# Performance work log

Hardware: AMD Instinct MI355X
Metric: run time of the kernel (lower is better)

The kernel has to match this reference:

```python
import jax, jax.numpy as jnp
import numpy as np

EMB = 1024
HEADS = 16
WINDOW = 128


def setup_inputs() -> dict:
    key = jax.random.key(0)
    ks = jax.random.split(key, 9)
    B, N = 2, 2048
    s = 0.02
    f32 = jnp.float32
    return {
        "x": jax.random.normal(ks[0], (B, N, EMB), dtype=f32),
        "Wq": jax.random.normal(ks[1], (EMB, EMB), dtype=f32) * s,
        "bq": jnp.zeros((EMB,), dtype=f32),
        "Wk": jax.random.normal(ks[2], (EMB, EMB), dtype=f32) * s,
        "bk": jnp.zeros((EMB,), dtype=f32),
        "Wv": jax.random.normal(ks[3], (EMB, EMB), dtype=f32) * s,
        "bv": jnp.zeros((EMB,), dtype=f32),
        "Wp": jax.random.normal(ks[4], (EMB, EMB), dtype=f32) * s,
        "bp": jnp.zeros((EMB,), dtype=f32),
    }


def reference(x, Wq, bq, Wk, bk, Wv, bv, Wp, bp):
    B, N, E = x.shape
    H = HEADS
    d = E // H

    def proj(W, b):
        # torch nn.Linear: y = x @ W^T + b, then split heads -> [b, h, n, d]
        y = jnp.einsum('bne,fe->bnf', x, W) + b
        return y.reshape(B, N, H, d).transpose(0, 2, 1, 3)

    q = proj(Wq, bq)
    k = proj(Wk, bk)
    v = proj(Wv, bv)

    # full QK^T then mask out-of-window entries (faithful to original)
    energy = jnp.einsum('bhqd,bhkd->bhqk', q, k)  # [B,H,N,N]
    idx = jnp.arange(N)
    out_of_window = jnp.abs(idx[:, None] - idx[None, :]) > WINDOW  # [N,N] bool
    fmin = jnp.finfo(jnp.float32).min
    energy = jnp.where(out_of_window, fmin, energy)

    scaling = jnp.sqrt(jnp.float32(E))  # note: original scales by sqrt(emb_size)
    att = jax.nn.softmax(energy / scaling, axis=-1)

    out = jnp.einsum('bhqk,bhkd->bhqd', att, v)  # [B,H,N,d]
    out = out.transpose(0, 2, 1, 3).reshape(B, N, E)
    return jnp.einsum('bne,fe->bnf', out, Wp) + bp
```

## Files before the change

kernel.cpp:

```cpp
#include <hip/hip_runtime.h>
#include <stdint.h>

#define EMB    1024
#define NHEAD  16
#define HDIM   64
#define NSEQ   2048
#define NBATCH 2
#define WINDOW 128
#define MROWS  (NBATCH * NSEQ)

typedef __attribute__((ext_vector_type(8))) short  bf16x8;
typedef __attribute__((ext_vector_type(4))) float  f32x4;
typedef __attribute__((ext_vector_type(4))) short  short4v;

__device__ __forceinline__ unsigned short f2bf(float f) {
  union { float f; uint32_t u; } c; c.f = f;
  uint32_t u = c.u;
  u += 0x7fffu + ((u >> 16) & 1u);
  return (unsigned short)(u >> 16);
}

#define GLOAD16(g, l) __builtin_amdgcn_global_load_lds( \
    (const __attribute__((address_space(1))) void*)(g), \
    (__attribute__((address_space(3))) void*)(l), 16, 0, 0)

__global__ __launch_bounds__(256) void cvt_all(
    const float* __restrict__ x,
    const float* __restrict__ w0, const float* __restrict__ w1,
    const float* __restrict__ w2, const float* __restrict__ w3,
    unsigned short* __restrict__ xb,
    unsigned short* __restrict__ o0, unsigned short* __restrict__ o1,
    unsigned short* __restrict__ o2, unsigned short* __restrict__ o3) {
  const int i = blockIdx.x * 256 + threadIdx.x;
  const float* src; unsigned short* dst; int off;
  if (i < 1048576) { src = x; dst = xb; off = i; }
  else {
    int j = i - 1048576;
    int sel = j >> 18; off = j & 262143;
    src = sel == 0 ? w0 : sel == 1 ? w1 : sel == 2 ? w2 : w3;
    dst = sel == 0 ? o0 : sel == 1 ? o1 : sel == 2 ? o2 : o3;
  }
  float4 v = ((const float4*)src)[off];
  short4v o;
  o.x = (short)f2bf(v.x);
  o.y = (short)f2bf(v.y);
  o.z = (short)f2bf(v.z);
  o.w = (short)f2bf(v.w);
  ((short4v*)dst)[off] = o;
}

__device__ __forceinline__ void gemm_pipe(const unsigned short* __restrict__ A,
                                          const unsigned short* __restrict__ Bw,
                                          const float* __restrict__ bias,
                                          void* __restrict__ Cv,
                                          int m0, int n0, int mode, float scale) {
  constexpr int K = 1024, BK = 64, NT = K / BK;
  __shared__ char lds[2][32768];
  const int t    = threadIdx.x;
  const int lane = t & 63;
  const int wv   = t >> 6;
  const int lhi  = lane >> 4, llo = lane & 15;
  const int wr   = wv >> 1, wc = wv & 1;

  const unsigned short* gsrc[8];
  int ldsoff[8];
  #pragma unroll
  for (int li = 0; li < 8; ++li) {
    const int isB = li >= 4;
    const int c = (isB ? (li - 4) : li) * 4 + wv;
    const int P = c * 1024 + lane * 16;
    const int L = P ^ (((P >> 7) & 7) << 4);
    const int row = L >> 7, sl = (L >> 4) & 7;
    gsrc[li] = (isB ? Bw + (size_t)(n0 + row) * K : A + (size_t)(m0 + row) * K) + sl * 8;
    ldsoff[li] = isB * 16384 + c * 1024;
  }

  int aoff[2][4], boff[2][4];
  #pragma unroll
  for (int ks = 0; ks < 2; ++ks)
    #pragma unroll
    for (int f = 0; f < 4; ++f) {
      const int ar = wr * 64 + f * 16 + llo;
      aoff[ks][f] = (ar * 128 + ks * 64 + lhi * 16) ^ ((ar & 7) << 4);
      const int bc = wc * 64 + f * 16 + llo;
      boff[ks][f] = 16384 + ((bc * 128 + ks * 64 + lhi * 16) ^ ((bc & 7) << 4));
    }

  const f32x4 zero = {0.f, 0.f, 0.f, 0.f};
  f32x4 acc[4][4];
  #pragma unroll
  for (int i = 0; i < 4; ++i)
    #pragma unroll
    for (int j = 0; j < 4; ++j) acc[i][j] = zero;

  #pragma unroll
  for (int li = 0; li < 8; ++li) GLOAD16(gsrc[li], (char*)lds + ldsoff[li]);
  #pragma unroll
  for (int li = 0; li < 8; ++li) GLOAD16(gsrc[li] + BK, (char*)lds + 32768 + ldsoff[li]);

  for (int t0 = 0; t0 < NT; ++t0) {
    if (t0 + 1 < NT) asm volatile("s_waitcnt vmcnt(8)" ::: "memory");
    else             asm volatile("s_waitcnt vmcnt(0)" ::: "memory");
    asm volatile("s_barrier" ::: "memory");
    __builtin_amdgcn_sched_barrier(0);

    const char* base = (const char*)lds + (t0 & 1) * 32768;
    bf16x8 af[2][4], bg[2][4];
    #pragma unroll
    for (int ks = 0; ks < 2; ++ks)
      #pragma unroll
      for (int f = 0; f < 4; ++f) {
        af[ks][f] = *(const bf16x8*)(base + aoff[ks][f]);
        bg[ks][f] = *(const bf16x8*)(base + boff[ks][f]);
      }
    asm volatile("s_waitcnt lgkmcnt(0)" ::: "memory");
    asm volatile("s_barrier" ::: "memory");
    __builtin_amdgcn_sched_barrier(0);

    if (t0 + 2 < NT) {
      #pragma unroll
      for (int li = 0; li < 8; ++li)
        GLOAD16(gsrc[li] + (t0 + 2) * BK, (char*)lds + (t0 & 1) * 32768 + ldsoff[li]);
    }

    __builtin_amdgcn_s_setprio(1);
    #pragma unroll
    for (int ks = 0; ks < 2; ++ks)
      #pragma unroll
      for (int mf = 0; mf < 4; ++mf)
        #pragma unroll
        for (int nf = 0; nf < 4; ++nf)
          acc[mf][nf] = __builtin_amdgcn_mfma_f32_16x16x32_bf16(af[ks][mf], bg[ks][nf], acc[mf][nf], 0, 0, 0);
    __builtin_amdgcn_s_setprio(0);
  }

  const int wm = wr * 64, wn = wc * 64;
  #pragma unroll
  for (int mf = 0; mf < 4; ++mf) {
    #pragma unroll
    for (int nf = 0; nf < 4; ++nf) {
      const int col = n0 + wn + nf * 16 + llo;
      if (mode == 1) {
        const int row_base = m0 + wm + mf * 16 + lhi * 4;
        const int bb = row_base >> 11, n = row_base & 2047;
        const int hh = col >> 6, dd = col & 63;
        short4v o;
        #pragma unroll
        for (int r = 0; r < 4; ++r) o[r] = (short)f2bf((acc[mf][nf][r] + bias[col]) * scale);
        unsigned short* p = (unsigned short*)Cv +
            ((size_t)((bb * NHEAD + hh) * HDIM + dd)) * NSEQ + n;
        *(short4v*)p = o;
      } else {
        #pragma unroll
        for (int r = 0; r < 4; ++r) {
          const int row = m0 + wm + mf * 16 + lhi * 4 + r;
          const float v = (acc[mf][nf][r] + bias[col]) * scale;
          if (mode == 0) {
            const int bb = row >> 11, n = row & 2047;
            const int hh = col >> 6, dd = col & 63;
            ((unsigned short*)Cv)[((size_t)(bb * NHEAD + hh) * NSEQ + n) * HDIM + dd] = f2bf(v);
          } else {
            ((float*)Cv)[(size_t)row * EMB + col] = v;
          }
        }
      }
    }
  }
}

__global__ __launch_bounds__(256, 2) void gemm_qkv(
    const unsigned short* __restrict__ A,
    const unsigned short* __restrict__ W0, const unsigned short* __restrict__ W1,
    const unsigned short* __restrict__ W2,
    const float* __restrict__ b0, const float* __restrict__ b1, const float* __restrict__ b2,
    unsigned short* __restrict__ O0, unsigned short* __restrict__ O1,
    unsigned short* __restrict__ O2) {
  const int m0 = blockIdx.x * 128, n0 = blockIdx.y * 128;
  const unsigned short* W = (blockIdx.z == 0) ? W0 : (blockIdx.z == 1) ? W1 : W2;
  const float* bb         = (blockIdx.z == 0) ? b0 : (blockIdx.z == 1) ? b1 : b2;
  unsigned short* O       = (blockIdx.z == 0) ? O0 : (blockIdx.z == 1) ? O1 : O2;
  const int mode          = (blockIdx.z == 2) ? 1 : 0;
  const float scale       = (blockIdx.z == 0) ? 0.03125f : 1.0f;
  gemm_pipe(A, W, bb, (void*)O, m0, n0, mode, scale);
}

__global__ __launch_bounds__(256, 2) void gemm_proj(
    const unsigned short* __restrict__ A, const unsigned short* __restrict__ W,
    const float* __restrict__ bias, float* __restrict__ O) {
  gemm_pipe(A, W, bias, (void*)O, blockIdx.x * 128, blockIdx.y * 128, 2, 1.0f);
}

__global__ __launch_bounds__(256, 4) void attn_kernel(
    const unsigned short* __restrict__ Qh, const unsigned short* __restrict__ Kh,
    const unsigned short* __restrict__ Vt, unsigned short* __restrict__ AO) {
  constexpr int NCH = 5;
  __shared__ char kv[2][16384];
  __shared__ unsigned short Pb[4][1024];
  const int t = threadIdx.x;
  const int lane = t & 63, wv = t >> 6;
  const int lhi = lane >> 4, llo = lane & 15;

  const int linear = blockIdx.x + 32 * (blockIdx.y + 16 * blockIdx.z);
  const int xcd = linear & 7, pos = linear >> 3;
  const int plane = xcd * 4 + (pos >> 5);
  const int qblk = pos & 31;
  const int b = plane >> 4, h = plane & 15;
  const int q0b = qblk * 64;
  const int q0 = q0b + wv * 16;

  const size_t pbase = (size_t)plane * NSEQ * HDIM;

  bf16x8 aq0, aq1;
  {
    const unsigned short* qp = Qh + pbase + (size_t)(q0 + llo) * HDIM + 8 * lhi;
    aq0 = *(const bf16x8*)qp;
    aq1 = *(const bf16x8*)(qp + 32);
  }

  int srow[4], scol8[4];
  #pragma unroll
  for (int li = 0; li < 4; ++li) {
    const int P = (li & 1) * 4096 + t * 16;
    const int L = P ^ (((P >> 7) & 7) << 4);
    srow[li] = L >> 7;
    scol8[li] = ((L >> 4) & 7) * 8;
  }

  int koff[4];
  #pragma unroll
  for (int half = 0; half < 4; ++half) {
    const int row = half * 16 + llo;
    koff[half] = (row * 128 + lhi * 16) ^ ((row & 7) << 4);
  }
  int voff[4][2];
  #pragma unroll
  for (int fd = 0; fd < 4; ++fd) {
    const int row = fd * 16 + llo;
    #pragma unroll
    for (int ks = 0; ks < 2; ++ks)
      voff[fd][ks] = 8192 + ((row * 128 + ks * 64 + lhi * 16) ^ ((row & 7) << 4));
  }
  int paoff[2];
  #pragma unroll
  for (int ks = 0; ks < 2; ++ks)
    paoff[ks] = (llo * 128 + ks * 64 + lhi * 16) ^ ((llo & 7) << 4);
  char* pb = (char*)&Pb[wv][0];

  bf16x8 vones;
  #pragma unroll
  for (int j = 0; j < 8; ++j) vones[j] = (short)0x3F80;

  const f32x4 zero = {0.f, 0.f, 0.f, 0.f};
  f32x4 accv[4];
  f32x4 s_acc = zero;
  #pragma unroll
  for (int i = 0; i < 4; ++i) accv[i] = zero;

  auto stage = [&](int ct, int slot) {
    const int kb = q0b - WINDOW + ct * 64;
    #pragma unroll
    for (int li = 0; li < 2; ++li) {
      int n = kb + srow[li];
      n = n < 0 ? 0 : (n > NSEQ - 1 ? NSEQ - 1 : n);
      GLOAD16(Kh + pbase + (size_t)n * HDIM + scol8[li],
              (char*)kv[slot] + (li & 1) * 4096 + t * 16);
    }
    #pragma unroll
    for (int li = 2; li < 4; ++li) {
      int c = kb + scol8[li];
      c = c < 0 ? 0 : (c > NSEQ - 8 ? NSEQ - 8 : c);
      GLOAD16(Vt + pbase + (size_t)srow[li] * NSEQ + c,
              (char*)kv[slot] + 8192 + (li & 1) * 4096 + t * 16);
    }
  };

  stage(0, 0);
  stage(1, 1);

  for (int ct = 0; ct < NCH; ++ct) {
    if (ct + 1 < NCH) asm volatile("s_waitcnt vmcnt(4)" ::: "memory");
    else              asm volatile("s_waitcnt vmcnt(0)" ::: "memory");
    asm volatile("s_barrier" ::: "memory");
    __builtin_amdgcn_sched_barrier(0);

    const char* sb = kv[ct & 1];
    const int kb = q0b - WINDOW + ct * 64;

    f32x4 e[4];
    #pragma unroll
    for (int half = 0; half < 4; ++half) {
      bf16x8 k0 = *(const bf16x8*)(sb + koff[half]);
      bf16x8 k1 = *(const bf16x8*)(sb + (koff[half] ^ 64));
      f32x4 z = zero;
      z = __builtin_amdgcn_mfma_f32_16x16x32_bf16(aq0, k0, z, 0, 0, 0);
      z = __builtin_amdgcn_mfma_f32_16x16x32_bf16(aq1, k1, z, 0, 0, 0);
      e[half] = z;
    }

    #pragma unroll
    for (int half = 0; half < 4; ++half) {
      const int key = kb + half * 16 + llo;
      #pragma unroll
      for (int r = 0; r < 4; ++r) {
        const int q = q0 + lhi * 4 + r;
        const int dlt = key - q;
        const bool valid = (key >= 0) && (key < NSEQ) && (dlt <= WINDOW) && (dlt >= -WINDOW);
        const float p = __expf(valid ? fminf(e[half][r], 40.f) : -1e30f);
        const int row = lhi * 4 + r, col = half * 16 + llo;
        *(unsigned short*)(pb + ((row * 128 + col * 2) ^ ((row & 7) << 4))) = f2bf(p);
      }
    }
    const bf16x8 pa0 = *(const bf16x8*)(pb + paoff[0]);
    const bf16x8 pa1 = *(const bf16x8*)(pb + paoff[1]);

    bf16x8 bv[4][2];
    #pragma unroll
    for (int fd = 0; fd < 4; ++fd) {
      bv[fd][0] = *(const bf16x8*)(sb + voff[fd][0]);
      bv[fd][1] = *(const bf16x8*)(sb + voff[fd][1]);
    }
    asm volatile("s_waitcnt lgkmcnt(0)" ::: "memory");
    __builtin_amdgcn_sched_barrier(0);
    asm volatile("s_barrier" ::: "memory");
    __builtin_amdgcn_sched_barrier(0);

    if (ct + 2 < NCH) stage(ct + 2, ct & 1);

    __builtin_amdgcn_s_setprio(1);
    s_acc = __builtin_amdgcn_mfma_f32_16x16x32_bf16(pa0, vones, s_acc, 0, 0, 0);
    s_acc = __builtin_amdgcn_mfma_f32_16x16x32_bf16(pa1, vones, s_acc, 0, 0, 0);
    #pragma unroll
    for (int fd = 0; fd < 4; ++fd) {
      accv[fd] = __builtin_amdgcn_mfma_f32_16x16x32_bf16(pa0, bv[fd][0], accv[fd], 0, 0, 0);
      accv[fd] = __builtin_amdgcn_mfma_f32_16x16x32_bf16(pa1, bv[fd][1], accv[fd], 0, 0, 0);
    }
    __builtin_amdgcn_s_setprio(0);
  }

  #pragma unroll
  for (int fd = 0; fd < 4; ++fd) {
    #pragma unroll
    for (int r = 0; r < 4; ++r) {
      const float o = accv[fd][r] / s_acc[r];
      const int q = q0 + lhi * 4 + r;
      AO[((size_t)b * NSEQ + q) * EMB + h * HDIM + fd * 16 + llo] = f2bf(o);
    }
  }
}

extern "C" void kernel_launch(void* const* d_in, const int* in_sizes, int n_in,
                              void* d_out, int out_size, void* d_ws, size_t ws_size,
                              hipStream_t stream) {
  (void)in_sizes; (void)n_in; (void)out_size; (void)ws_size;
  const float* x  = (const float*)d_in[0];
  const float* Wq = (const float*)d_in[1];
  const float* bq = (const float*)d_in[2];
  const float* Wk = (const float*)d_in[3];
  const float* bk = (const float*)d_in[4];
  const float* Wv = (const float*)d_in[5];
  const float* bv = (const float*)d_in[6];
  const float* Wp = (const float*)d_in[7];
  const float* bp = (const float*)d_in[8];
  float* out = (float*)d_out;
  char* ws = (char*)d_ws;
  const size_t MB = 1u << 20;
  unsigned short* xb  = (unsigned short*)(ws + 0 * MB);
  unsigned short* Wqb = (unsigned short*)(ws + 8 * MB);
  unsigned short* Wkb = (unsigned short*)(ws + 10 * MB);
  unsigned short* Wvb = (unsigned short*)(ws + 12 * MB);
  unsigned short* Wpb = (unsigned short*)(ws + 14 * MB);
  unsigned short* Qb  = (unsigned short*)(ws + 16 * MB);
  unsigned short* Kb  = (unsigned short*)(ws + 24 * MB);
  unsigned short* Vtb = (unsigned short*)(ws + 32 * MB);
  unsigned short* AOb = (unsigned short*)(ws + 40 * MB);

  cvt_all<<<dim3(8192), dim3(256), 0, stream>>>(x, Wq, Wk, Wv, Wp,
                                                xb, Wqb, Wkb, Wvb, Wpb);

  gemm_qkv<<<dim3(MROWS / 128, EMB / 128, 3), dim3(256), 0, stream>>>(
      xb, Wqb, Wkb, Wvb, bq, bk, bv, Qb, Kb, Vtb);

  attn_kernel<<<dim3(NSEQ / 64, NHEAD, NBATCH), dim3(256), 0, stream>>>(Qb, Kb, Vtb, AOb);

  gemm_proj<<<dim3(MROWS / 128, EMB / 128), dim3(256), 0, stream>>>(AOb, Wpb, bp, out);
}
```

Before: 78.94 us.

## Split GEMM k-step MFMAs across barrier and skip out-of-window attention sub-chunks

In the projection GEMM, the two k-substeps of LDS fragment loads are issued separately and the first substep's MFMAs run before the second's loads finish and before the buffer-release barrier, so LDS reads overlap with compute. In the windowed attention kernel, each 64-key chunk is split into two 32-key halves. Halves entirely outside the query block's window or the sequence bounds skip the QK^T, exp and PV MFMAs. The PV accumulation now runs before the barrier and the next stage's prefetch rather than after it, which lengthens the critical section between barriers and adds a divergent (wave-uniform) branch.

```diff
diff --git a/kernel.cpp b/kernel.cpp
--- a/kernel.cpp
+++ b/kernel.cpp
@@ -105,15 +105,31 @@
     __builtin_amdgcn_sched_barrier(0);
 
     const char* base = (const char*)lds + (t0 & 1) * 32768;
-    bf16x8 af[2][4], bg[2][4];
-    #pragma unroll
-    for (int ks = 0; ks < 2; ++ks)
+    bf16x8 af0[4], bg0[4], af1[4], bg1[4];
+    #pragma unroll
+    for (int f = 0; f < 4; ++f) {
+      af0[f] = *(const bf16x8*)(base + aoff[0][f]);
+      bg0[f] = *(const bf16x8*)(base + boff[0][f]);
+    }
+    __builtin_amdgcn_sched_barrier(0);
+    #pragma unroll
+    for (int f = 0; f < 4; ++f) {
+      af1[f] = *(const bf16x8*)(base + aoff[1][f]);
+      bg1[f] = *(const bf16x8*)(base + boff[1][f]);
+    }
+    asm volatile("s_waitcnt lgkmcnt(8)" ::: "memory");
+    __builtin_amdgcn_sched_barrier(0);
+
+    __builtin_amdgcn_s_setprio(1);
+    #pragma unroll
+    for (int mf = 0; mf < 4; ++mf)
       #pragma unroll
-      for (int f = 0; f < 4; ++f) {
-        af[ks][f] = *(const bf16x8*)(base + aoff[ks][f]);
-        bg[ks][f] = *(const bf16x8*)(base + boff[ks][f]);
-      }
+      for (int nf = 0; nf < 4; ++nf)
+        acc[mf][nf] = __builtin_amdgcn_mfma_f32_16x16x32_bf16(af0[mf], bg0[nf], acc[mf][nf], 0, 0, 0);
+    __builtin_amdgcn_s_setprio(0);
+
     asm volatile("s_waitcnt lgkmcnt(0)" ::: "memory");
+    __builtin_amdgcn_sched_barrier(0);
     asm volatile("s_barrier" ::: "memory");
     __builtin_amdgcn_sched_barrier(0);
 
@@ -125,12 +141,10 @@
 
     __builtin_amdgcn_s_setprio(1);
     #pragma unroll
-    for (int ks = 0; ks < 2; ++ks)
+    for (int mf = 0; mf < 4; ++mf)
       #pragma unroll
-      for (int mf = 0; mf < 4; ++mf)
-        #pragma unroll
-        for (int nf = 0; nf < 4; ++nf)
-          acc[mf][nf] = __builtin_amdgcn_mfma_f32_16x16x32_bf16(af[ks][mf], bg[ks][nf], acc[mf][nf], 0, 0, 0);
+      for (int nf = 0; nf < 4; ++nf)
+        acc[mf][nf] = __builtin_amdgcn_mfma_f32_16x16x32_bf16(af1[mf], bg1[nf], acc[mf][nf], 0, 0, 0);
     __builtin_amdgcn_s_setprio(0);
   }
 
@@ -286,55 +300,64 @@
     const char* sb = kv[ct & 1];
     const int kb = q0b - WINDOW + ct * 64;
 
-    f32x4 e[4];
-    #pragma unroll
-    for (int half = 0; half < 4; ++half) {
-      bf16x8 k0 = *(const bf16x8*)(sb + koff[half]);
-      bf16x8 k1 = *(const bf16x8*)(sb + (koff[half] ^ 64));
-      f32x4 z = zero;
-      z = __builtin_amdgcn_mfma_f32_16x16x32_bf16(aq0, k0, z, 0, 0, 0);
-      z = __builtin_amdgcn_mfma_f32_16x16x32_bf16(aq1, k1, z, 0, 0, 0);
-      e[half] = z;
-    }
-
-    #pragma unroll
-    for (int half = 0; half < 4; ++half) {
-      const int key = kb + half * 16 + llo;
-      #pragma unroll
-      for (int r = 0; r < 4; ++r) {
-        const int q = q0 + lhi * 4 + r;
-        const int dlt = key - q;
-        const bool valid = (key >= 0) && (key < NSEQ) && (dlt <= WINDOW) && (dlt >= -WINDOW);
-        const float p = __expf(valid ? fminf(e[half][r], 40.f) : -1e30f);
-        const int row = lhi * 4 + r, col = half * 16 + llo;
-        *(unsigned short*)(pb + ((row * 128 + col * 2) ^ ((row & 7) << 4))) = f2bf(p);
+    #pragma unroll
+    for (int ks = 0; ks < 2; ++ks) {
+      const int kbs = kb + ks * 32;
+      const bool active = (kbs <= q0 + 143) && (kbs + 31 >= q0 - 128) &&
+                          (kbs < NSEQ) && (kbs + 31 >= 0);
+      if (active) {
+        f32x4 e0, e1;
+        {
+          bf16x8 k0 = *(const bf16x8*)(sb + koff[2 * ks]);
+          bf16x8 k1 = *(const bf16x8*)(sb + (koff[2 * ks] ^ 64));
+          f32x4 z = zero;
+          z = __builtin_amdgcn_mfma_f32_16x16x32_bf16(aq0, k0, z, 0, 0, 0);
+          z = __builtin_amdgcn_mfma_f32_16x16x32_bf16(aq1, k1, z, 0, 0, 0);
+          e0 = z;
+        }
+        {
+          bf16x8 k0 = *(const bf16x8*)(sb + koff[2 * ks + 1]);
+          bf16x8 k1 = *(const bf16x8*)(sb + (koff[2 * ks + 1] ^ 64));
+          f32x4 z = zero;
+          z = __builtin_amdgcn_mfma_f32_16x16x32_bf16(aq0, k0, z, 0, 0, 0);
+          z = __builtin_amdgcn_mfma_f32_16x16x32_bf16(aq1, k1, z, 0, 0, 0);
+          e1 = z;
+        }
+        #pragma unroll
+        for (int hf = 0; hf < 2; ++hf) {
+          const int half = 2 * ks + hf;
+          const int key = kb + half * 16 + llo;
+          #pragma unroll
+          for (int r = 0; r < 4; ++r) {
+            const int q = q0 + lhi * 4 + r;
+            const int dlt = key - q;
+            const bool valid = (key >= 0) && (key < NSEQ) && (dlt <= WINDOW) && (dlt >= -WINDOW);
+            const float ev = valid ? fminf((hf == 0 ? e0[r] : e1[r]), 40.f) : -1e30f;
+            const float p = __expf(ev);
+            const int row = lhi * 4 + r, col = half * 16 + llo;
+            *(unsigned short*)(pb + ((row * 128 + col * 2) ^ ((row & 7) << 4))) = f2bf(p);
+          }
+        }
+        const bf16x8 pa = *(const bf16x8*)(pb + paoff[ks]);
+        bf16x8 bv[4];
+        #pragma unroll
+        for (int fd = 0; fd < 4; ++fd) bv[fd] = *(const bf16x8*)(sb + voff[fd][ks]);
+
+        __builtin_amdgcn_s_setprio(1);
+        s_acc = __builtin_amdgcn_mfma_f32_16x16x32_bf16(pa, vones, s_acc, 0, 0, 0);
+        #pragma unroll
+        for (int fd = 0; fd < 4; ++fd)
+          accv[fd] = __builtin_amdgcn_mfma_f32_16x16x32_bf16(pa, bv[fd], accv[fd], 0, 0, 0);
+        __builtin_amdgcn_s_setprio(0);
       }
     }
-    const bf16x8 pa0 = *(const bf16x8*)(pb + paoff[0]);
-    const bf16x8 pa1 = *(const bf16x8*)(pb + paoff[1]);
-
-    bf16x8 bv[4][2];
-    #pragma unroll
-    for (int fd = 0; fd < 4; ++fd) {
-      bv[fd][0] = *(const bf16x8*)(sb + voff[fd][0]);
-      bv[fd][1] = *(const bf16x8*)(sb + voff[fd][1]);
-    }
+
     asm volatile("s_waitcnt lgkmcnt(0)" ::: "memory");
     __builtin_amdgcn_sched_barrier(0);
     asm volatile("s_barrier" ::: "memory");
     __builtin_amdgcn_sched_barrier(0);
 
     if (ct + 2 < NCH) stage(ct + 2, ct & 1);
-
-    __builtin_amdgcn_s_setprio(1);
-    s_acc = __builtin_amdgcn_mfma_f32_16x16x32_bf16(pa0, vones, s_acc, 0, 0, 0);
-    s_acc = __builtin_amdgcn_mfma_f32_16x16x32_bf16(pa1, vones, s_acc, 0, 0, 0);
-    #pragma unroll
-    for (int fd = 0; fd < 4; ++fd) {
-      accv[fd] = __builtin_amdgcn_mfma_f32_16x16x32_bf16(pa0, bv[fd][0], accv[fd], 0, 0, 0);
-      accv[fd] = __builtin_amdgcn_mfma_f32_16x16x32_bf16(pa1, bv[fd][1], accv[fd], 0, 0, 0);
-    }
-    __builtin_amdgcn_s_setprio(0);
   }
 
   #pragma unroll
```

Result: no change. 80.09 us (+1.5%).

## Replace QKV GEMM with 256x256-tile, 8-wave pipelined kernel and XCD-aware block remap

Applied to the files above, without the earlier changes.

The fused QKV projection moves from 128x128 tiles with 256 threads to a dedicated 256x256-tile kernel with 512 threads (8 waves), using half-tile staged global-to-LDS loads interleaved between four MFMA phases per K step. Block indices are remapped so neighbouring tiles land on the same XCD. The aim is more data reuse per LDS byte and better overlap of loads with MFMA work. The cost is 128KB of LDS per block and only 192 blocks, which fills the device less evenly. The output projection keeps the old pipeline, specialised to fp32 output.

```diff
diff --git a/kernel.cpp b/kernel.cpp
--- a/kernel.cpp
+++ b/kernel.cpp
@@ -9,9 +9,9 @@
 #define WINDOW 128
 #define MROWS  (NBATCH * NSEQ)
 
-typedef __attribute__((ext_vector_type(8))) short  bf16x8;
-typedef __attribute__((ext_vector_type(4))) float  f32x4;
-typedef __attribute__((ext_vector_type(4))) short  short4v;
+typedef __attribute__((ext_vector_type(8)))  short  bf16x8;
+typedef __attribute__((ext_vector_type(4)))  float  f32x4;
+typedef __attribute__((ext_vector_type(4)))  short  short4v;
 
 __device__ __forceinline__ unsigned short f2bf(float f) {
   union { float f; uint32_t u; } c; c.f = f;
@@ -49,13 +49,197 @@
   ((short4v*)dst)[off] = o;
 }
 
-__device__ __forceinline__ void gemm_pipe(const unsigned short* __restrict__ A,
-                                          const unsigned short* __restrict__ Bw,
-                                          const float* __restrict__ bias,
-                                          void* __restrict__ Cv,
-                                          int m0, int n0, int mode, float scale) {
+__global__ __launch_bounds__(512, 2) void gemm_qkv256(
+    const unsigned short* __restrict__ A,
+    const unsigned short* __restrict__ W0, const unsigned short* __restrict__ W1,
+    const unsigned short* __restrict__ W2,
+    const float* __restrict__ b0p, const float* __restrict__ b1p, const float* __restrict__ b2p,
+    unsigned short* __restrict__ O0, unsigned short* __restrict__ O1,
+    unsigned short* __restrict__ O2) {
+  constexpr int K = 1024, NT = 16;
+  __shared__ char lds[2][65536];
+  const int t = threadIdx.x;
+  const int lane = t & 63, wv = t >> 6;
+  const int lhi = lane >> 4, llo = lane & 15;
+  const int wr = wv >> 2, wc = wv & 3;
+
+  const int orig = blockIdx.x + 16 * (blockIdx.y + 4 * blockIdx.z);
+  const int tl = (orig & 7) * 24 + (orig >> 3);
+  const int by = tl & 3, bx = (tl >> 2) & 15, bz = tl >> 6;
+  const int m0 = bx * 256, n0 = by * 256;
+  const unsigned short* Bw = bz == 0 ? W0 : bz == 1 ? W1 : W2;
+  const float* bias        = bz == 0 ? b0p : bz == 1 ? b1p : b2p;
+  unsigned short* Cv       = bz == 0 ? O0 : bz == 1 ? O1 : O2;
+  const int   mode  = (bz == 2) ? 1 : 0;
+  const float scale = (bz == 0) ? 0.03125f : 1.0f;
+
+  const int srow0 = t >> 3, srow1 = 64 + (t >> 3);
+  const int scol8 = ((t & 7) ^ ((t >> 3) & 7)) * 8;
+  const unsigned short* pA0 = A  + (size_t)m0 * K;
+  const unsigned short* pA1 = A  + (size_t)(m0 + 128) * K;
+  const unsigned short* pB0 = Bw + (size_t)n0 * K;
+  const unsigned short* pB1 = Bw + (size_t)(n0 + 128) * K;
+
+  auto stageH = [&](const unsigned short* base, int kt, char* dst) {
+    GLOAD16(base + (size_t)srow0 * K + kt * 64 + scol8, dst + t * 16);
+    GLOAD16(base + (size_t)srow1 * K + kt * 64 + scol8, dst + 8192 + t * 16);
+  };
+
+  int aoff[8];
+  #pragma unroll
+  for (int mf = 0; mf < 8; ++mf) {
+    const int lr = (mf & 3) * 16 + wr * 64 + llo;
+    aoff[mf] = (mf >> 2) * 16384 + ((lr * 128 + lhi * 16) ^ ((lr & 7) << 4));
+  }
+  int boff[4];
+  #pragma unroll
+  for (int nf = 0; nf < 4; ++nf) {
+    const int lc = (nf & 1) * 16 + wc * 32 + llo;
+    boff[nf] = 32768 + (nf >> 1) * 16384 + ((lc * 128 + lhi * 16) ^ ((lc & 7) << 4));
+  }
+
+  const f32x4 zero = {0.f, 0.f, 0.f, 0.f};
+  f32x4 acc[8][4];
+  #pragma unroll
+  for (int i = 0; i < 8; ++i)
+    #pragma unroll
+    for (int j = 0; j < 4; ++j) acc[i][j] = zero;
+
+  stageH(pA0, 0, (char*)lds[0]);
+  stageH(pB0, 0, (char*)lds[0] + 32768);
+  stageH(pA1, 0, (char*)lds[0] + 16384);
+  stageH(pB1, 0, (char*)lds[0] + 49152);
+  stageH(pA0, 1, (char*)lds[1]);
+  stageH(pB0, 1, (char*)lds[1] + 32768);
+  __builtin_amdgcn_sched_barrier(0);
+  asm volatile("s_waitcnt vmcnt(8)" ::: "memory");
+  asm volatile("s_barrier" ::: "memory");
+  __builtin_amdgcn_sched_barrier(0);
+
+  for (int ti = 0; ti < NT; ++ti) {
+    char* cur = (char*)lds[ti & 1];
+    char* nxt = (char*)lds[(ti + 1) & 1];
+    bf16x8 aF[4][2], bF0[2][2], bF1[2][2];
+
+    #pragma unroll
+    for (int mf = 0; mf < 4; ++mf) {
+      aF[mf][0] = *(const bf16x8*)(cur + aoff[mf]);
+      aF[mf][1] = *(const bf16x8*)(cur + (aoff[mf] ^ 64));
+    }
+    #pragma unroll
+    for (int nf = 0; nf < 2; ++nf) {
+      bF0[nf][0] = *(const bf16x8*)(cur + boff[nf]);
+      bF0[nf][1] = *(const bf16x8*)(cur + (boff[nf] ^ 64));
+    }
+    asm volatile("s_waitcnt lgkmcnt(0)" ::: "memory");
+    __builtin_amdgcn_sched_barrier(0);
+    if (ti + 1 < NT) { stageH(pA1, ti + 1, nxt + 16384); __builtin_amdgcn_sched_barrier(0); }
+    if (ti + 1 < NT) asm volatile("s_waitcnt vmcnt(6)" ::: "memory");
+    else             asm volatile("s_waitcnt vmcnt(0)" ::: "memory");
+    asm volatile("s_barrier" ::: "memory");
+    __builtin_amdgcn_sched_barrier(0);
+    __builtin_amdgcn_s_setprio(1);
+    #pragma unroll
+    for (int mf = 0; mf < 4; ++mf)
+      #pragma unroll
+      for (int nf = 0; nf < 2; ++nf)
+        #pragma unroll
+        for (int ks = 0; ks < 2; ++ks)
+          acc[mf][nf] = __builtin_amdgcn_mfma_f32_16x16x32_bf16(aF[mf][ks], bF0[nf][ks], acc[mf][nf], 0, 0, 0);
+    __builtin_amdgcn_s_setprio(0);
+
+    #pragma unroll
+    for (int nf = 0; nf < 2; ++nf) {
+      bF1[nf][0] = *(const bf16x8*)(cur + boff[nf + 2]);
+      bF1[nf][1] = *(const bf16x8*)(cur + (boff[nf + 2] ^ 64));
+    }
+    asm volatile("s_waitcnt lgkmcnt(0)" ::: "memory");
+    __builtin_amdgcn_sched_barrier(0);
+    if (ti + 1 < NT) { stageH(pB1, ti + 1, nxt + 49152); __builtin_amdgcn_sched_barrier(0); }
+    asm volatile("s_barrier" ::: "memory");
+    __builtin_amdgcn_sched_barrier(0);
+    __builtin_amdgcn_s_setprio(1);
+    #pragma unroll
+    for (int mf = 0; mf < 4; ++mf)
+      #pragma unroll
+      for (int nf = 0; nf < 2; ++nf)
+        #pragma unroll
+        for (int ks = 0; ks < 2; ++ks)
+          acc[mf][nf + 2] = __builtin_amdgcn_mfma_f32_16x16x32_bf16(aF[mf][ks], bF1[nf][ks], acc[mf][nf + 2], 0, 0, 0);
+    __builtin_amdgcn_s_setprio(0);
+
+    #pragma unroll
+    for (int mf = 0; mf < 4; ++mf) {
+      aF[mf][0] = *(const bf16x8*)(cur + aoff[mf + 4]);
+      aF[mf][1] = *(const bf16x8*)(cur + (aoff[mf + 4] ^ 64));
+    }
+    asm volatile("s_waitcnt lgkmcnt(0)" ::: "memory");
+    __builtin_amdgcn_sched_barrier(0);
+    if (ti + 2 < NT) { stageH(pA0, ti + 2, cur); __builtin_amdgcn_sched_barrier(0); }
+    asm volatile("s_barrier" ::: "memory");
+    __builtin_amdgcn_sched_barrier(0);
+    __builtin_amdgcn_s_setprio(1);
+    #pragma unroll
+    for (int mf = 0; mf < 4; ++mf)
+      #pragma unroll
+      for (int nf = 0; nf < 2; ++nf)
+        #pragma unroll
+        for (int ks = 0; ks < 2; ++ks)
+          acc[mf + 4][nf] = __builtin_amdgcn_mfma_f32_16x16x32_bf16(aF[mf][ks], bF0[nf][ks], acc[mf + 4][nf], 0, 0, 0);
+    __builtin_amdgcn_s_setprio(0);
+
+    if (ti + 2 < NT) { stageH(pB0, ti + 2, cur + 32768); __builtin_amdgcn_sched_barrier(0); }
+    if (ti + 2 < NT)      asm volatile("s_waitcnt vmcnt(8)" ::: "memory");
+    else if (ti + 1 < NT) asm volatile("s_waitcnt vmcnt(4)" ::: "memory");
+    else                  asm volatile("s_waitcnt vmcnt(0)" ::: "memory");
+    asm volatile("s_barrier" ::: "memory");
+    __builtin_amdgcn_sched_barrier(0);
+    __builtin_amdgcn_s_setprio(1);
+    #pragma unroll
+    for (int mf = 0; mf < 4; ++mf)
+      #pragma unroll
+      for (int nf = 0; nf < 2; ++nf)
+        #pragma unroll
+        for (int ks = 0; ks < 2; ++ks)
+          acc[mf + 4][nf + 2] = __builtin_amdgcn_mfma_f32_16x16x32_bf16(aF[mf][ks], bF1[nf][ks], acc[mf + 4][nf + 2], 0, 0, 0);
+    __builtin_amdgcn_s_setprio(0);
+  }
+
+  #pragma unroll
+  for (int mf = 0; mf < 8; ++mf) {
+    const int rowb = m0 + (mf >> 2) * 128 + wr * 64 + (mf & 3) * 16 + lhi * 4;
+    #pragma unroll
+    for (int nf = 0; nf < 4; ++nf) {
+      const int col = n0 + (nf >> 1) * 128 + wc * 32 + (nf & 1) * 16 + llo;
+      const float bcol = bias[col];
+      if (mode == 1) {
+        const int bb = rowb >> 11, n = rowb & 2047;
+        const int hh = col >> 6, dd = col & 63;
+        short4v o;
+        #pragma unroll
+        for (int r = 0; r < 4; ++r) o[r] = (short)f2bf(acc[mf][nf][r] + bcol);
+        unsigned short* p = Cv + ((size_t)((bb * NHEAD + hh) * HDIM + dd)) * NSEQ + n;
+        *(short4v*)p = o;
+      } else {
+        #pragma unroll
+        for (int r = 0; r < 4; ++r) {
+          const int row = rowb + r;
+          const float v = (acc[mf][nf][r] + bcol) * scale;
+          const int bb = row >> 11, n = row & 2047;
+          const int hh = col >> 6, dd = col & 63;
+          Cv[((size_t)(bb * NHEAD + hh) * NSEQ + n) * HDIM + dd] = f2bf(v);
+        }
+      }
+    }
+  }
+}
+
+__global__ __launch_bounds__(256, 2) void gemm_proj(
+    const unsigned short* __restrict__ A, const unsigned short* __restrict__ Bw,
+    const float* __restrict__ bias, float* __restrict__ Cv) {
   constexpr int K = 1024, BK = 64, NT = K / BK;
   __shared__ char lds[2][32768];
+  const int m0 = blockIdx.x * 128, n0 = blockIdx.y * 128;
   const int t    = threadIdx.x;
   const int lane = t & 63;
   const int wv   = t >> 6;
@@ -140,54 +324,13 @@
     #pragma unroll
     for (int nf = 0; nf < 4; ++nf) {
       const int col = n0 + wn + nf * 16 + llo;
-      if (mode == 1) {
-        const int row_base = m0 + wm + mf * 16 + lhi * 4;
-        const int bb = row_base >> 11, n = row_base & 2047;
-        const int hh = col >> 6, dd = col & 63;
-        short4v o;
-        #pragma unroll
-        for (int r = 0; r < 4; ++r) o[r] = (short)f2bf((acc[mf][nf][r] + bias[col]) * scale);
-        unsigned short* p = (unsigned short*)Cv +
-            ((size_t)((bb * NHEAD + hh) * HDIM + dd)) * NSEQ + n;
-        *(short4v*)p = o;
-      } else {
-        #pragma unroll
-        for (int r = 0; r < 4; ++r) {
-          const int row = m0 + wm + mf * 16 + lhi * 4 + r;
-          const float v = (acc[mf][nf][r] + bias[col]) * scale;
-          if (mode == 0) {
-            const int bb = row >> 11, n = row & 2047;
-            const int hh = col >> 6, dd = col & 63;
-            ((unsigned short*)Cv)[((size_t)(bb * NHEAD + hh) * NSEQ + n) * HDIM + dd] = f2bf(v);
-          } else {
-            ((float*)Cv)[(size_t)row * EMB + col] = v;
-          }
-        }
+      #pragma unroll
+      for (int r = 0; r < 4; ++r) {
+        const int row = m0 + wm + mf * 16 + lhi * 4 + r;
+        Cv[(size_t)row * EMB + col] = acc[mf][nf][r] + bias[col];
       }
     }
   }
-}
-
-__global__ __launch_bounds__(256, 2) void gemm_qkv(
-    const unsigned short* __restrict__ A,
-    const unsigned short* __restrict__ W0, const unsigned short* __restrict__ W1,
-    const unsigned short* __restrict__ W2,
-    const float* __restrict__ b0, const float* __restrict__ b1, const float* __restrict__ b2,
-    unsigned short* __restrict__ O0, unsigned short* __restrict__ O1,
-    unsigned short* __restrict__ O2) {
-  const int m0 = blockIdx.x * 128, n0 = blockIdx.y * 128;
-  const unsigned short* W = (blockIdx.z == 0) ? W0 : (blockIdx.z == 1) ? W1 : W2;
-  const float* bb         = (blockIdx.z == 0) ? b0 : (blockIdx.z == 1) ? b1 : b2;
-  unsigned short* O       = (blockIdx.z == 0) ? O0 : (blockIdx.z == 1) ? O1 : O2;
-  const int mode          = (blockIdx.z == 2) ? 1 : 0;
-  const float scale       = (blockIdx.z == 0) ? 0.03125f : 1.0f;
-  gemm_pipe(A, W, bb, (void*)O, m0, n0, mode, scale);
-}
-
-__global__ __launch_bounds__(256, 2) void gemm_proj(
-    const unsigned short* __restrict__ A, const unsigned short* __restrict__ W,
-    const float* __restrict__ bias, float* __restrict__ O) {
-  gemm_pipe(A, W, bias, (void*)O, blockIdx.x * 128, blockIdx.y * 128, 2, 1.0f);
 }
 
 __global__ __launch_bounds__(256, 4) void attn_kernel(
@@ -377,7 +520,7 @@
   cvt_all<<<dim3(8192), dim3(256), 0, stream>>>(x, Wq, Wk, Wv, Wp,
                                                 xb, Wqb, Wkb, Wvb, Wpb);
 
-  gemm_qkv<<<dim3(MROWS / 128, EMB / 128, 3), dim3(256), 0, stream>>>(
+  gemm_qkv256<<<dim3(16, 4, 3), dim3(512), 0, stream>>>(
       xb, Wqb, Wkb, Wvb, bq, bk, bv, Qb, Kb, Vtb);
 
   attn_kernel<<<dim3(NSEQ / 64, NHEAD, NBATCH), dim3(256), 0, stream>>>(Qb, Kb, Vtb, AOb);
```

Result: no change. 80.41 us (+1.9%).

## Widen attention blocks to 128 queries and skip out-of-window key chunks per wave

Applied to the files above, without the earlier changes.

The attention kernel now uses 512-thread blocks covering 128 queries and walks 6 shared K/V chunks instead of 5. Each staged K/V tile is reused by 8 waves rather than 4, which cuts redundant global loads of the window. Each wave skips its QK, softmax and PV work on chunks that lie outside its own window. In exchange there are fewer blocks in the grid, each thread issues fewer loads per stage, and the divergent skip has to stay consistent with the barriers.

```diff
diff --git a/kernel.cpp b/kernel.cpp
--- a/kernel.cpp
+++ b/kernel.cpp
@@ -190,22 +190,22 @@
   gemm_pipe(A, W, bias, (void*)O, blockIdx.x * 128, blockIdx.y * 128, 2, 1.0f);
 }
 
-__global__ __launch_bounds__(256, 4) void attn_kernel(
+__global__ __launch_bounds__(512, 2) void attn_kernel(
     const unsigned short* __restrict__ Qh, const unsigned short* __restrict__ Kh,
     const unsigned short* __restrict__ Vt, unsigned short* __restrict__ AO) {
-  constexpr int NCH = 5;
+  constexpr int NCH = 6;
   __shared__ char kv[2][16384];
-  __shared__ unsigned short Pb[4][1024];
+  __shared__ unsigned short Pb[8][1024];
   const int t = threadIdx.x;
   const int lane = t & 63, wv = t >> 6;
   const int lhi = lane >> 4, llo = lane & 15;
 
-  const int linear = blockIdx.x + 32 * (blockIdx.y + 16 * blockIdx.z);
+  const int linear = blockIdx.x + 16 * (blockIdx.y + 16 * blockIdx.z);
   const int xcd = linear & 7, pos = linear >> 3;
-  const int plane = xcd * 4 + (pos >> 5);
-  const int qblk = pos & 31;
+  const int plane = xcd * 4 + (pos >> 4);
+  const int qblk = pos & 15;
   const int b = plane >> 4, h = plane & 15;
-  const int q0b = qblk * 64;
+  const int q0b = qblk * 128;
   const int q0 = q0b + wv * 16;
 
   const size_t pbase = (size_t)plane * NSEQ * HDIM;
@@ -217,14 +217,10 @@
     aq1 = *(const bf16x8*)(qp + 32);
   }
 
-  int srow[4], scol8[4];
-  #pragma unroll
-  for (int li = 0; li < 4; ++li) {
-    const int P = (li & 1) * 4096 + t * 16;
-    const int L = P ^ (((P >> 7) & 7) << 4);
-    srow[li] = L >> 7;
-    scol8[li] = ((L >> 4) & 7) * 8;
-  }
+  const int SP = t * 16;
+  const int SL = SP ^ (((SP >> 7) & 7) << 4);
+  const int srow = SL >> 7;
+  const int scol8 = ((SL >> 4) & 7) * 8;
 
   int koff[4];
   #pragma unroll
@@ -258,66 +254,60 @@
 
   auto stage = [&](int ct, int slot) {
     const int kb = q0b - WINDOW + ct * 64;
-    #pragma unroll
-    for (int li = 0; li < 2; ++li) {
-      int n = kb + srow[li];
-      n = n < 0 ? 0 : (n > NSEQ - 1 ? NSEQ - 1 : n);
-      GLOAD16(Kh + pbase + (size_t)n * HDIM + scol8[li],
-              (char*)kv[slot] + (li & 1) * 4096 + t * 16);
-    }
-    #pragma unroll
-    for (int li = 2; li < 4; ++li) {
-      int c = kb + scol8[li];
-      c = c < 0 ? 0 : (c > NSEQ - 8 ? NSEQ - 8 : c);
-      GLOAD16(Vt + pbase + (size_t)srow[li] * NSEQ + c,
-              (char*)kv[slot] + 8192 + (li & 1) * 4096 + t * 16);
-    }
+    int n = kb + srow;
+    n = n < 0 ? 0 : (n > NSEQ - 1 ? NSEQ - 1 : n);
+    GLOAD16(Kh + pbase + (size_t)n * HDIM + scol8, (char*)kv[slot] + SP);
+    int c = kb + scol8;
+    c = c < 0 ? 0 : (c > NSEQ - 8 ? NSEQ - 8 : c);
+    GLOAD16(Vt + pbase + (size_t)srow * NSEQ + c, (char*)kv[slot] + 8192 + SP);
   };
 
   stage(0, 0);
   stage(1, 1);
 
   for (int ct = 0; ct < NCH; ++ct) {
-    if (ct + 1 < NCH) asm volatile("s_waitcnt vmcnt(4)" ::: "memory");
+    if (ct + 1 < NCH) asm volatile("s_waitcnt vmcnt(2)" ::: "memory");
     else              asm volatile("s_waitcnt vmcnt(0)" ::: "memory");
     asm volatile("s_barrier" ::: "memory");
     __builtin_amdgcn_sched_barrier(0);
 
     const char* sb = kv[ct & 1];
     const int kb = q0b - WINDOW + ct * 64;
-
-    f32x4 e[4];
-    #pragma unroll
-    for (int half = 0; half < 4; ++half) {
-      bf16x8 k0 = *(const bf16x8*)(sb + koff[half]);
-      bf16x8 k1 = *(const bf16x8*)(sb + (koff[half] ^ 64));
-      f32x4 z = zero;
-      z = __builtin_amdgcn_mfma_f32_16x16x32_bf16(aq0, k0, z, 0, 0, 0);
-      z = __builtin_amdgcn_mfma_f32_16x16x32_bf16(aq1, k1, z, 0, 0, 0);
-      e[half] = z;
-    }
-
-    #pragma unroll
-    for (int half = 0; half < 4; ++half) {
-      const int key = kb + half * 16 + llo;
-      #pragma unroll
-      for (int r = 0; r < 4; ++r) {
-        const int q = q0 + lhi * 4 + r;
-        const int dlt = key - q;
-        const bool valid = (key >= 0) && (key < NSEQ) && (dlt <= WINDOW) && (dlt >= -WINDOW);
-        const float p = __expf(valid ? fminf(e[half][r], 40.f) : -1e30f);
-        const int row = lhi * 4 + r, col = half * 16 + llo;
-        *(unsigned short*)(pb + ((row * 128 + col * 2) ^ ((row & 7) << 4))) = f2bf(p);
-      }
-    }
-    const bf16x8 pa0 = *(const bf16x8*)(pb + paoff[0]);
-    const bf16x8 pa1 = *(const bf16x8*)(pb + paoff[1]);
-
-    bf16x8 bv[4][2];
-    #pragma unroll
-    for (int fd = 0; fd < 4; ++fd) {
-      bv[fd][0] = *(const bf16x8*)(sb + voff[fd][0]);
-      bv[fd][1] = *(const bf16x8*)(sb + voff[fd][1]);
+    const bool active = (kb <= q0 + 143) && (kb + 63 >= q0 - 128) &&
+                        (kb < NSEQ) && (kb + 63 >= 0);
+
+    bf16x8 pa0, pa1, bv[4][2];
+    if (active) {
+      f32x4 e[4];
+      #pragma unroll
+      for (int half = 0; half < 4; ++half) {
+        bf16x8 k0 = *(const bf16x8*)(sb + koff[half]);
+        bf16x8 k1 = *(const bf16x8*)(sb + (koff[half] ^ 64));
+        f32x4 z = zero;
+        z = __builtin_amdgcn_mfma_f32_16x16x32_bf16(aq0, k0, z, 0, 0, 0);
+        z = __builtin_amdgcn_mfma_f32_16x16x32_bf16(aq1, k1, z, 0, 0, 0);
+        e[half] = z;
+      }
+      #pragma unroll
+      for (int half = 0; half < 4; ++half) {
+        const int key = kb + half * 16 + llo;
+        #pragma unroll
+        for (int r = 0; r < 4; ++r) {
+          const int q = q0 + lhi * 4 + r;
+          const int dlt = key - q;
+          const bool valid = (key >= 0) && (key < NSEQ) && (dlt <= WINDOW) && (dlt >= -WINDOW);
+          const float p = __expf(valid ? fminf(e[half][r], 40.f) : -1e30f);
+          const int row = lhi * 4 + r, col = half * 16 + llo;
+          *(unsigned short*)(pb + ((row * 128 + col * 2) ^ ((row & 7) << 4))) = f2bf(p);
+        }
+      }
+      pa0 = *(const bf16x8*)(pb + paoff[0]);
+      pa1 = *(const bf16x8*)(pb + paoff[1]);
+      #pragma unroll
+      for (int fd = 0; fd < 4; ++fd) {
+        bv[fd][0] = *(const bf16x8*)(sb + voff[fd][0]);
+        bv[fd][1] = *(const bf16x8*)(sb + voff[fd][1]);
+      }
     }
     asm volatile("s_waitcnt lgkmcnt(0)" ::: "memory");
     __builtin_amdgcn_sched_barrier(0);
@@ -326,15 +316,17 @@
 
     if (ct + 2 < NCH) stage(ct + 2, ct & 1);
 
-    __builtin_amdgcn_s_setprio(1);
-    s_acc = __builtin_amdgcn_mfma_f32_16x16x32_bf16(pa0, vones, s_acc, 0, 0, 0);
-    s_acc = __builtin_amdgcn_mfma_f32_16x16x32_bf16(pa1, vones, s_acc, 0, 0, 0);
-    #pragma unroll
-    for (int fd = 0; fd < 4; ++fd) {
-      accv[fd] = __builtin_amdgcn_mfma_f32_16x16x32_bf16(pa0, bv[fd][0], accv[fd], 0, 0, 0);
-      accv[fd] = __builtin_amdgcn_mfma_f32_16x16x32_bf16(pa1, bv[fd][1], accv[fd], 0, 0, 0);
-    }
-    __builtin_amdgcn_s_setprio(0);
+    if (active) {
+      __builtin_amdgcn_s_setprio(1);
+      s_acc = __builtin_amdgcn_mfma_f32_16x16x32_bf16(pa0, vones, s_acc, 0, 0, 0);
+      s_acc = __builtin_amdgcn_mfma_f32_16x16x32_bf16(pa1, vones, s_acc, 0, 0, 0);
+      #pragma unroll
+      for (int fd = 0; fd < 4; ++fd) {
+        accv[fd] = __builtin_amdgcn_mfma_f32_16x16x32_bf16(pa0, bv[fd][0], accv[fd], 0, 0, 0);
+        accv[fd] = __builtin_amdgcn_mfma_f32_16x16x32_bf16(pa1, bv[fd][1], accv[fd], 0, 0, 0);
+      }
+      __builtin_amdgcn_s_setprio(0);
+    }
   }
 
   #pragma unroll
@@ -380,7 +372,7 @@
   gemm_qkv<<<dim3(MROWS / 128, EMB / 128, 3), dim3(256), 0, stream>>>(
       xb, Wqb, Wkb, Wvb, bq, bk, bv, Qb, Kb, Vtb);
 
-  attn_kernel<<<dim3(NSEQ / 64, NHEAD, NBATCH), dim3(256), 0, stream>>>(Qb, Kb, Vtb, AOb);
+  attn_kernel<<<dim3(NSEQ / 128, NHEAD, NBATCH), dim3(512), 0, stream>>>(Qb, Kb, Vtb, AOb);
 
   gemm_proj<<<dim3(MROWS / 128, EMB / 128), dim3(256), 0, stream>>>(AOb, Wpb, bp, out);
 }
```

Result: slower. 80.54 us (+2.0%).
